# Performance work log

Hardware: AMD Instinct MI355X
Metric: run time of the kernel (lower is better)

## Reference

```python
import jax, jax.numpy as jnp
import numpy as np

N = 20000      # nodes
E = 320000     # edges (before self loops)
IN = 128       # in_channels
HID = 256      # hidden_channels
HEADS = 8
C = HID // HEADS  # 32 per-head dim
L = 4          # num_gat_layers
BN_EPS = 1e-5
LN_EPS = 1e-5


def setup_inputs() -> dict:
    key = jax.random.key(0)
    ks = iter(jax.random.split(key, 64))
    def rn(shape, s=0.05):
        return jax.random.normal(next(ks), shape, jnp.float32) * s
    inp = {
        'x': jax.random.normal(next(ks), (N, IN), jnp.float32),
        'edge_index': jax.random.randint(next(ks), (2, E), 0, N),
        # FeatureMLP
        'mlp_w1': rn((IN, HID)), 'mlp_b1': jnp.zeros((HID,), jnp.float32),
        'bn1_g': jnp.ones((HID,), jnp.float32), 'bn1_b': jnp.zeros((HID,), jnp.float32),
        'mlp_w2': rn((HID, HID)), 'mlp_b2': jnp.zeros((HID,), jnp.float32),
        'bn2_g': jnp.ones((HID,), jnp.float32), 'bn2_b': jnp.zeros((HID,), jnp.float32),
        'mlp_w3': rn((HID, HID)), 'mlp_b3': jnp.zeros((HID,), jnp.float32),
        # stacked GATv2 layer params [L, ...]
        'gat_wl': rn((L, HID, HID)), 'gat_bl': jnp.zeros((L, HID), jnp.float32),
        'gat_wr': rn((L, HID, HID)), 'gat_br': jnp.zeros((L, HID), jnp.float32),
        'gat_att': rn((L, HEADS, C)), 'gat_bias': jnp.zeros((L, HID), jnp.float32),
        'ln_g': jnp.ones((L, HID), jnp.float32), 'ln_b': jnp.zeros((L, HID), jnp.float32),
        'head_w1': rn((2 * HID, HID)), 'head_b1': jnp.zeros((HID,), jnp.float32),
        'hbn1_g': jnp.ones((HID,), jnp.float32), 'hbn1_b': jnp.zeros((HID,), jnp.float32),
        'head_w2': rn((HID, HID // 2)), 'head_b2': jnp.zeros((HID // 2,), jnp.float32),
        'hbn2_g': jnp.ones((HID // 2,), jnp.float32), 'hbn2_b': jnp.zeros((HID // 2,), jnp.float32),
        'head_w3': rn((HID // 2, HID // 4)), 'head_b3': jnp.zeros((HID // 4,), jnp.float32),
        'head_w4': rn((HID // 4, 1)), 'head_b4': jnp.zeros((1,), jnp.float32),
    }
    return inp


def _lrelu01(v):
    return jax.nn.leaky_relu(v, 0.1)


def _bn_eval(v, g, b):
    # eval-mode BatchNorm1d with running_mean=0, running_var=1
    return v * (g / jnp.sqrt(1.0 + BN_EPS)) + b


def _layernorm(v, g, b):
    mu = jnp.mean(v, axis=-1, keepdims=True)
    var = jnp.mean((v - mu) ** 2, axis=-1, keepdims=True)
    return (v - mu) / jnp.sqrt(var + LN_EPS) * g + b


def _gatv2(x, src, dst, Wl, bl, Wr, br, att, bias):
    n = x.shape[0]
    xl = (x @ Wl + bl).reshape(n, HEADS, C)   # source transform
    xr = (x @ Wr + br).reshape(n, HEADS, C)   # target transform
    # per-edge attention logits (GATv2): a . LeakyReLU(x_l[src] + x_r[dst])
    e = jax.nn.leaky_relu(xl[src] + xr[dst], 0.2)          # [E, H, C]
    logits = jnp.einsum('ehc,hc->eh', e, att)               # [E, H]
    # segment softmax over destination nodes
    m = jax.ops.segment_max(logits, dst, num_segments=n)    # [N, H]
    a = jnp.exp(logits - m[dst])
    s = jax.ops.segment_sum(a, dst, num_segments=n)
    alpha = a / (s[dst] + 1e-16)                            # [E, H]
    out = jax.ops.segment_sum(xl[src] * alpha[:, :, None], dst, num_segments=n)
    return out.reshape(n, HID) + bias


def _forward(x, mlp_w1, mlp_b1, bn1_g, bn1_b, mlp_w2, mlp_b2, bn2_g, bn2_b,
             mlp_w3, mlp_b3, gat_wl, gat_bl, gat_wr, gat_br, gat_att, gat_bias,
             ln_g, ln_b, head_w1, head_b1, hbn1_g, hbn1_b, head_w2, head_b2,
             hbn2_g, hbn2_b, head_w3, head_b3, head_w4, head_b4, edge_index):
    n = x.shape[0]
    # FeatureMLP (eval: dropout off)
    h = _lrelu01(_bn_eval(x @ mlp_w1 + mlp_b1, bn1_g, bn1_b))
    h = _lrelu01(_bn_eval(h @ mlp_w2 + mlp_b2, bn2_g, bn2_b))
    x_mlp = h @ mlp_w3 + mlp_b3
    # add self loops
    loop = jnp.arange(n)
    src = jnp.concatenate([edge_index[0], loop])
    dst = jnp.concatenate([edge_index[1], loop])
    g = x_mlp
    for i in range(L):
        res = g
        o = _gatv2(g, src, dst, gat_wl[i], gat_bl[i], gat_wr[i], gat_br[i],
                   gat_att[i], gat_bias[i])
        o = _lrelu01(_layernorm(o, ln_g[i], ln_b[i]))
        g = o + res
    xc = jnp.concatenate([x_mlp, g], axis=1)                # [N, 2*HID]
    h = _lrelu01(_bn_eval(xc @ head_w1 + head_b1, hbn1_g, hbn1_b))
    h = _lrelu01(_bn_eval(h @ head_w2 + head_b2, hbn2_g, hbn2_b))
    h = _lrelu01(h @ head_w3 + head_b3)
    return h @ head_w4 + head_b4                            # [N, 1]


def reference(x, edge_index, mlp_w1, mlp_b1, bn1_g, bn1_b, mlp_w2, mlp_b2,
              bn2_g, bn2_b, mlp_w3, mlp_b3, gat_wl, gat_bl, gat_wr, gat_br,
              gat_att, gat_bias, ln_g, ln_b, head_w1, head_b1, hbn1_g, hbn1_b,
              head_w2, head_b2, hbn2_g, hbn2_b, head_w3, head_b3, head_w4, head_b4):
    return _forward(x, mlp_w1, mlp_b1, bn1_g, bn1_b, mlp_w2, mlp_b2, bn2_g,
                    bn2_b, mlp_w3, mlp_b3, gat_wl, gat_bl, gat_wr, gat_br,
                    gat_att, gat_bias, ln_g, ln_b, head_w1, head_b1, hbn1_g,
                    hbn1_b, head_w2, head_b2, hbn2_g, hbn2_b, head_w3, head_b3,
                    head_w4, head_b4, edge_index)
```

## Files before the change

kernel.cpp:

```cpp
#include <hip/hip_runtime.h>
#include <hip/hip_bf16.h>

#define N_NODES 20000
#define E_EDGES 320000
#define E_TOT   (E_EDGES + N_NODES)
#define IN_CH   128
#define HID     256
#define HEADS   8
#define CPH     32

enum { EP_BIAS = 0, EP_BN_LRELU = 1, EP_LRELU = 2 };

typedef _Float16 f16;
typedef f16  f16x2 __attribute__((ext_vector_type(2)));
typedef f16  f16x4 __attribute__((ext_vector_type(4)));
typedef f16  f16x8 __attribute__((ext_vector_type(8)));
typedef float f32x2 __attribute__((ext_vector_type(2)));
typedef float f32x4 __attribute__((ext_vector_type(4)));

__device__ __forceinline__ f16x2 h2max(f16x2 a, f16x2 b) {
#if __has_builtin(__builtin_elementwise_max)
    return __builtin_elementwise_max(a, b);
#else
    f16x2 r; r[0] = a[0] > b[0] ? a[0] : b[0]; r[1] = a[1] > b[1] ? a[1] : b[1]; return r;
#endif
}
__device__ __forceinline__ float hdot2(f16x2 a, f16x2 b, float c) {
#if __has_builtin(__builtin_amdgcn_fdot2)
    return __builtin_amdgcn_fdot2(a, b, c, false);
#else
    return c + (float)a[0] * (float)b[0] + (float)a[1] * (float)b[1];
#endif
}
__device__ __forceinline__ float fexp2(float x) {
#if __has_builtin(__builtin_amdgcn_exp2f)
    return __builtin_amdgcn_exp2f(x);
#else
    return exp2f(x);
#endif
}

__device__ __forceinline__ size_t frag_idx(int row, int col, int KB) {
    int kb = col >> 6, ks = (col >> 5) & 1, q = (col >> 3) & 3, e = col & 7;
    return ((((size_t)(row >> 4) * KB + kb) * 2 + ks) << 9) + (((q << 4) | (row & 15)) << 3) + e;
}

struct WDesc { const float* src; f16* dst; int K; int Nc; int NTOT; int ct0; };
struct WDescs { WDesc d[14]; };

#define WPREP_BLKS (14 * 512)
#define CVT_BLKS   ((N_NODES * IN_CH) / 256)
#define DEG_BLKS   ((E_EDGES + 255) / 256)
#define ZERO_BLKS  ((N_NODES + 255) / 256)
#define PREP_BLKS  (WPREP_BLKS + CVT_BLKS + DEG_BLKS + ZERO_BLKS)

__global__ __launch_bounds__(256)
void prep_kernel(WDescs ds, const float* __restrict__ x, f16* __restrict__ x16,
                 const int* __restrict__ dstE, int* __restrict__ cnt, int* __restrict__ cur)
{
    const int bx = blockIdx.x;
    const int tid = threadIdx.x;
    if (bx < WPREP_BLKS) {
        WDesc w = ds.d[bx >> 9];
        int i = ((bx & 511) << 8) + tid;
        if (i < w.K * w.Nc) {
            int NT_local = w.Nc >> 4;
            int e  = i & 7;
            int l  = (i >> 3) & 63;
            int r  = i >> 9;
            int ct = r % NT_local;
            int q  = r / NT_local;
            int ks = q & 1;
            int kb = q >> 1;
            int n  = ct * 16 + (l & 15);
            int k  = kb * 64 + ks * 32 + ((l >> 4) << 3) + e;
            size_t di = (((size_t)(kb * 2 + ks) * w.NTOT + w.ct0 + ct) << 9) + (l << 3) + e;
            w.dst[di] = (f16)w.src[(size_t)k * w.Nc + n];
        }
    } else if (bx < WPREP_BLKS + CVT_BLKS) {
        int i = (bx - WPREP_BLKS) * 256 + tid;
        if (i < N_NODES * IN_CH) {
            int row = i / IN_CH, col = i - row * IN_CH;
            x16[frag_idx(row, col, 2)] = (f16)x[i];
        }
    } else if (bx < WPREP_BLKS + CVT_BLKS + DEG_BLKS) {
        int e = (bx - WPREP_BLKS - CVT_BLKS) * 256 + tid;
        if (e < E_EDGES) atomicAdd(&cnt[dstE[e]], 1);
    } else {
        int i = (bx - WPREP_BLKS - CVT_BLKS - DEG_BLKS) * 256 + tid;
        if (i < N_NODES) cur[i] = 0;
    }
}

template<int NT, int NTOT, int WAVES, int RT, int DOT, int OUTF>
__global__ __launch_bounds__(WAVES * 64)
void gemm_kernel(const f16* __restrict__ A1, int KB1,
                 const f16* __restrict__ A2, int KB2,
                 const f16* __restrict__ Wf,
                 const float* __restrict__ biasA,
                 const float* __restrict__ biasB,
                 const float* __restrict__ bng,
                 const float* __restrict__ bnb,
                 f16* __restrict__ out16A,
                 f16* __restrict__ out16B,
                 f16* __restrict__ dup16,
                 float* __restrict__ out32,
                 const float* __restrict__ dotw,
                 const float* __restrict__ dotb,
                 float* __restrict__ outdot,
                 int NcA, int KBo, int mode)
{
    __shared__ float red[DOT ? 16 : 1][DOT ? 65 : 1];
    const int tid  = threadIdx.x;
    const int wave = tid >> 6;
    const int lane = tid & 63;
    const int quad = lane >> 4;
    const int rb0 = blockIdx.x * RT;
    const int KBt = KB1 + KB2;

    f32x4 acc[RT][NT];
#pragma unroll
    for (int t = 0; t < RT; ++t)
#pragma unroll
        for (int j = 0; j < NT; ++j) acc[t][j] = (f32x4){0.f, 0.f, 0.f, 0.f};

#pragma unroll 2
    for (int kb = 0; kb < KBt; ++kb) {
#pragma unroll
        for (int ks = 0; ks < 2; ++ks) {
            f16x8 a[RT];
#pragma unroll
            for (int t = 0; t < RT; ++t) {
                const f16* ap = (kb < KB1)
                    ? A1 + (((((size_t)(rb0 + t)) * KB1 + kb) * 2 + ks) << 9) + (lane << 3)
                    : A2 + (((((size_t)(rb0 + t)) * KB2 + (kb - KB1)) * 2 + ks) << 9) + (lane << 3);
                a[t] = *(const f16x8*)ap;
            }
            const f16* bp = Wf + (((size_t)(kb * 2 + ks) * NTOT + wave * NT) << 9) + (lane << 3);
#pragma unroll
            for (int ct = 0; ct < NT; ++ct) {
                f16x8 b = *(const f16x8*)(bp + ((size_t)ct << 9));
#pragma unroll
                for (int t = 0; t < RT; ++t)
                    acc[t][ct] = __builtin_amdgcn_mfma_f32_16x16x32_f16(a[t], b, acc[t][ct], 0, 0, 0);
            }
        }
    }

    const int c0 = lane & 15;
    const int NcB = NTOT * 16 - NcA;
#pragma unroll
    for (int t = 0; t < RT; ++t) {
        const int r0 = (rb0 + t) * 16 + (quad << 2);
#pragma unroll
        for (int ct = 0; ct < NT; ++ct) {
            int col = (wave * NT + ct) * 16 + c0;
            bool isB = col >= NcA;
            int colL = isB ? col - NcA : col;
            float bv = isB ? biasB[colL] : biasA[colL];
            float sc = 1.f, sh = 0.f;
            if (mode == EP_BN_LRELU) {
                sc = bng[col] * rsqrtf(1.f + 1e-5f);
                sh = bnb[col];
            }
#pragma unroll
            for (int reg = 0; reg < 4; ++reg) {
                int row = r0 + reg;
                float v = acc[t][ct][reg] + bv;
                if (mode == EP_BN_LRELU) { v = v * sc + sh; v = v > 0.f ? v : 0.1f * v; }
                else if (mode == EP_LRELU) { v = v > 0.f ? v : 0.1f * v; }
                if (DOT) {
                    red[(quad << 2) + reg][col] = v * dotw[col];
                } else {
                    if (OUTF) {
                        size_t idx = frag_idx(row, col, KBo);
                        out16A[idx] = (f16)v;
                        if (dup16) dup16[idx] = (f16)v;
                        if (out32) out32[(size_t)row * NcA + col] = v;
                    } else {
                        f16* Cout = isB ? out16B : out16A;
                        int stride = isB ? NcB : NcA;
                        Cout[(size_t)row * stride + colL] = (f16)v;
                    }
                }
            }
        }
    }

    if (DOT) {
        __syncthreads();
        if (wave == 0) {
            int r = lane & 15, q = lane >> 4;
            float psum = 0.f;
#pragma unroll
            for (int j = 0; j < 16; ++j) psum += red[r][q * 16 + j];
            psum += __shfl_xor(psum, 16, 64);
            psum += __shfl_xor(psum, 32, 64);
            if (lane < 16) outdot[rb0 * 16 + r] = psum + dotb[0];
        }
    }
}

__global__ __launch_bounds__(512)
void head23_kernel(const f16* __restrict__ h1,
                   const f16* __restrict__ w2f,
                   const float* __restrict__ b2,
                   const float* __restrict__ bn2g, const float* __restrict__ bn2b,
                   const f16* __restrict__ w3f,
                   const float* __restrict__ b3,
                   const float* __restrict__ w4, const float* __restrict__ b4,
                   float* __restrict__ out)
{
    __shared__ f16  hs[32 * 136];
    __shared__ float red[32][65];
    const int tid  = threadIdx.x;
    const int wave = tid >> 6;
    const int lane = tid & 63;
    const int quad = lane >> 4;
    const int c0   = lane & 15;
    const int rb0  = blockIdx.x * 2;

    {
        f32x4 acc[2];
        acc[0] = (f32x4){0.f, 0.f, 0.f, 0.f};
        acc[1] = (f32x4){0.f, 0.f, 0.f, 0.f};
#pragma unroll
        for (int kb = 0; kb < 4; ++kb) {
#pragma unroll
            for (int ks = 0; ks < 2; ++ks) {
                f16x8 a0 = *(const f16x8*)(h1 + (((((size_t)rb0)     * 4 + kb) * 2 + ks) << 9) + (lane << 3));
                f16x8 a1 = *(const f16x8*)(h1 + (((((size_t)rb0 + 1) * 4 + kb) * 2 + ks) << 9) + (lane << 3));
                f16x8 b  = *(const f16x8*)(w2f + (((size_t)(kb * 2 + ks) * 8 + wave) << 9) + (lane << 3));
                acc[0] = __builtin_amdgcn_mfma_f32_16x16x32_f16(a0, b, acc[0], 0, 0, 0);
                acc[1] = __builtin_amdgcn_mfma_f32_16x16x32_f16(a1, b, acc[1], 0, 0, 0);
            }
        }
        const int col = wave * 16 + c0;
        const float sc = bn2g[col] * rsqrtf(1.f + 1e-5f);
        const float sh = bn2b[col];
        const float bv = b2[col];
#pragma unroll
        for (int t = 0; t < 2; ++t) {
            const int r0 = t * 16 + (quad << 2);
#pragma unroll
            for (int reg = 0; reg < 4; ++reg) {
                float v = acc[t][reg] + bv;
                v = v * sc + sh;
                v = v > 0.f ? v : 0.1f * v;
                hs[(r0 + reg) * 136 + col] = (f16)v;
            }
        }
    }
    __syncthreads();

    {
        const int rbL = wave >> 2;
        const int ct3 = wave & 3;
        f32x4 acc = (f32x4){0.f, 0.f, 0.f, 0.f};
#pragma unroll
        for (int ksl = 0; ksl < 4; ++ksl) {
            const int arow = rbL * 16 + (lane & 15);
            f16x8 a = *(const f16x8*)&hs[arow * 136 + ksl * 32 + ((lane >> 4) << 3)];
            f16x8 b = *(const f16x8*)(w3f + (((size_t)(ksl * 4 + ct3)) << 9) + (lane << 3));
            acc = __builtin_amdgcn_mfma_f32_16x16x32_f16(a, b, acc, 0, 0, 0);
        }
        const int col = ct3 * 16 + c0;
        const float wv = w4[col];
        const float bv = b3[col];
        const int r0 = rbL * 16 + (quad << 2);
#pragma unroll
        for (int reg = 0; reg < 4; ++reg) {
            float v = acc[reg] + bv;
            v = v > 0.f ? v : 0.1f * v;
            red[r0 + reg][col] = v * wv;
        }
    }
    __syncthreads();

    {
        const int row = wave * 4 + (lane >> 4);
        float pr = red[row][c0] + red[row][c0 + 16] + red[row][c0 + 32] + red[row][c0 + 48];
        pr += __shfl_xor(pr, 1, 64);
        pr += __shfl_xor(pr, 2, 64);
        pr += __shfl_xor(pr, 4, 64);
        pr += __shfl_xor(pr, 8, 64);
        if (c0 == 0) out[blockIdx.x * 32 + row] = pr + b4[0];
    }
}

__global__ __launch_bounds__(1024)
void scan_kernel(const int* __restrict__ cnt, int* __restrict__ off) {
    __shared__ int wsum[16];
    const int tid = threadIdx.x, wv = tid >> 6, ln = tid & 63;
    const int base = tid * 20;
    int pre[20];
    int loc = 0;
#pragma unroll
    for (int j = 0; j < 20; ++j) {
        int i = base + j;
        int c = (i < N_NODES) ? cnt[i] + 1 : 0;
        pre[j] = loc;
        loc += c;
    }
    int s = loc;
#pragma unroll
    for (int d = 1; d < 64; d <<= 1) { int t = __shfl_up(s, d, 64); if (ln >= d) s += t; }
    if (ln == 63) wsum[wv] = s;
    __syncthreads();
    int woff = 0;
#pragma unroll
    for (int j = 0; j < 16; ++j) if (j < wv) woff += wsum[j];
    int excl = woff + s - loc;
#pragma unroll
    for (int j = 0; j < 20; ++j) {
        int i = base + j;
        if (i < N_NODES) off[i] = excl + pre[j];
    }
    if (tid == 1023) off[N_NODES] = woff + s;
}

__global__ void fill_kernel(const int* __restrict__ src, const int* __restrict__ dst,
                            const int* __restrict__ off, int* __restrict__ cur, int* __restrict__ csr) {
    int i = blockIdx.x * 256 + threadIdx.x;
    if (i < E_EDGES) {
        int d = dst[i];
        int pos = atomicAdd(&cur[d], 1);
        csr[off[d] + pos] = src[i];
    } else {
        int j = i - E_EDGES;
        if (j < N_NODES) csr[off[j + 1] - 1] = j;
    }
}

__global__ __launch_bounds__(256)
void gat_agg_kernel(const f16* __restrict__ xl, const f16* __restrict__ xr,
                    float* __restrict__ g, f16* __restrict__ g16,
                    const int* __restrict__ off, const int* __restrict__ csr,
                    const float* __restrict__ att,
                    const float* __restrict__ bias,
                    const float* __restrict__ lng,
                    const float* __restrict__ lnb)
{
    const int wv   = threadIdx.x >> 6;
    const int ln   = threadIdx.x & 63;
    const int half = ln >> 5;
    const int lp   = ln & 31;
    const int n    = blockIdx.x * 4 + wv;
    if (n >= N_NODES) return;

    const f16x8* xl8 = (const f16x8*)xl;
    f16x8 xrv = ((const f16x8*)xr)[n * 32 + lp];
    f16x2 xr0; xr0[0] = xrv[0]; xr0[1] = xrv[1];
    f16x2 xr1; xr1[0] = xrv[2]; xr1[1] = xrv[3];
    f16x2 xr2; xr2[0] = xrv[4]; xr2[1] = xrv[5];
    f16x2 xr3; xr3[0] = xrv[6]; xr3[1] = xrv[7];
    float4 af0 = ((const float4*)att)[lp * 2];
    float4 af1 = ((const float4*)att)[lp * 2 + 1];
    const float L2E = 1.44269504f;
    f16x2 av0; av0[0] = (f16)(af0.x * L2E); av0[1] = (f16)(af0.y * L2E);
    f16x2 av1; av1[0] = (f16)(af0.z * L2E); av1[1] = (f16)(af0.w * L2E);
    f16x2 av2; av2[0] = (f16)(af1.x * L2E); av2[1] = (f16)(af1.y * L2E);
    f16x2 av3; av3[0] = (f16)(af1.z * L2E); av3[1] = (f16)(af1.w * L2E);
    const f16x2 k02 = { (f16)0.2f, (f16)0.2f };

    float s = 0.f;
    float o0 = 0.f, o1 = 0.f, o2 = 0.f, o3 = 0.f, o4 = 0.f, o5 = 0.f, o6 = 0.f, o7 = 0.f;

    int p = off[n], end = off[n + 1];

    auto procv = [&](f16x8 xv, bool valid) {
        f16x2 x0; x0[0] = xv[0]; x0[1] = xv[1];
        f16x2 x1; x1[0] = xv[2]; x1[1] = xv[3];
        f16x2 x2; x2[0] = xv[4]; x2[1] = xv[5];
        f16x2 x3; x3[0] = xv[6]; x3[1] = xv[7];
        f16x2 v0 = x0 + xr0, v1 = x1 + xr1, v2 = x2 + xr2, v3 = x3 + xr3;
        v0 = h2max(v0, v0 * k02); v1 = h2max(v1, v1 * k02);
        v2 = h2max(v2, v2 * k02); v3 = h2max(v3, v3 * k02);
        float pr = hdot2(v0, av0, hdot2(v1, av1, hdot2(v2, av2, hdot2(v3, av3, 0.f))));
        pr += __shfl_xor(pr, 1, 64);
        pr += __shfl_xor(pr, 2, 64);
        float e = valid ? fexp2(pr) : 0.f;
        s += e;
        o0 = fmaf((float)xv[0], e, o0); o1 = fmaf((float)xv[1], e, o1);
        o2 = fmaf((float)xv[2], e, o2); o3 = fmaf((float)xv[3], e, o3);
        o4 = fmaf((float)xv[4], e, o4); o5 = fmaf((float)xv[5], e, o5);
        o6 = fmaf((float)xv[6], e, o6); o7 = fmaf((float)xv[7], e, o7);
    };
    auto proc = [&](int ep) {
        bool valid = ep < end;
        int sidx = csr[valid ? ep : end - 1];
        procv(xl8[(size_t)sidx * 32 + lp], valid);
    };

    for (; p + 16 <= end; p += 16) {
        int sA = csr[p +      half];
        int sB = csr[p + 2  + half];
        int sC = csr[p + 4  + half];
        int sD = csr[p + 6  + half];
        int sE = csr[p + 8  + half];
        int sF = csr[p + 10 + half];
        int sG = csr[p + 12 + half];
        int sH = csr[p + 14 + half];
        f16x8 rA = xl8[(size_t)sA * 32 + lp];
        f16x8 rB = xl8[(size_t)sB * 32 + lp];
        f16x8 rC = xl8[(size_t)sC * 32 + lp];
        f16x8 rD = xl8[(size_t)sD * 32 + lp];
        f16x8 rE = xl8[(size_t)sE * 32 + lp];
        f16x8 rF = xl8[(size_t)sF * 32 + lp];
        f16x8 rG = xl8[(size_t)sG * 32 + lp];
        f16x8 rH = xl8[(size_t)sH * 32 + lp];
        procv(rA, true); procv(rB, true); procv(rC, true); procv(rD, true);
        procv(rE, true); procv(rF, true); procv(rG, true); procv(rH, true);
    }
    for (; p + 8 <= end; p += 8) {
        int sA = csr[p +     half];
        int sB = csr[p + 2 + half];
        int sC = csr[p + 4 + half];
        int sD = csr[p + 6 + half];
        f16x8 rA = xl8[(size_t)sA * 32 + lp];
        f16x8 rB = xl8[(size_t)sB * 32 + lp];
        f16x8 rC = xl8[(size_t)sC * 32 + lp];
        f16x8 rD = xl8[(size_t)sD * 32 + lp];
        procv(rA, true); procv(rB, true); procv(rC, true); procv(rD, true);
    }
    for (; p + 4 <= end; p += 4) {
        int sA = csr[p +     half];
        int sB = csr[p + 2 + half];
        f16x8 rA = xl8[(size_t)sA * 32 + lp];
        f16x8 rB = xl8[(size_t)sB * 32 + lp];
        procv(rA, true); procv(rB, true);
    }
    for (; p < end; p += 2) proc(p + half);

    s  += __shfl_xor(s, 32, 64);
    o0 += __shfl_xor(o0, 32, 64); o1 += __shfl_xor(o1, 32, 64);
    o2 += __shfl_xor(o2, 32, 64); o3 += __shfl_xor(o3, 32, 64);
    o4 += __shfl_xor(o4, 32, 64); o5 += __shfl_xor(o5, 32, 64);
    o6 += __shfl_xor(o6, 32, 64); o7 += __shfl_xor(o7, 32, 64);

    const int lidx = lp * 2 + half;
    float q0 = half ? o4 : o0;
    float q1 = half ? o5 : o1;
    float q2 = half ? o6 : o2;
    float q3 = half ? o7 : o3;

    float inv = 1.f / (s + 1e-16f);
    float4 bi = ((const float4*)bias)[lidx];
    float y0 = q0 * inv + bi.x;
    float y1 = q1 * inv + bi.y;
    float y2 = q2 * inv + bi.z;
    float y3 = q3 * inv + bi.w;

    float s1 = y0 + y1 + y2 + y3;
    float s2 = y0 * y0 + y1 * y1 + y2 * y2 + y3 * y3;
#pragma unroll
    for (int d = 32; d; d >>= 1) { s1 += __shfl_xor(s1, d, 64); s2 += __shfl_xor(s2, d, 64); }
    float mu  = s1 * (1.f / HID);
    float ex2 = s2 * (1.f / HID);
    float rstd = rsqrtf(ex2 - mu * mu + 1e-5f);
    float4 lg = ((const float4*)lng)[lidx];
    float4 lb = ((const float4*)lnb)[lidx];
    float nv0 = (y0 - mu) * rstd * lg.x + lb.x; nv0 = nv0 > 0.f ? nv0 : 0.1f * nv0;
    float nv1 = (y1 - mu) * rstd * lg.y + lb.y; nv1 = nv1 > 0.f ? nv1 : 0.1f * nv1;
    float nv2 = (y2 - mu) * rstd * lg.z + lb.z; nv2 = nv2 > 0.f ? nv2 : 0.1f * nv2;
    float nv3 = (y3 - mu) * rstd * lg.w + lb.w; nv3 = nv3 > 0.f ? nv3 : 0.1f * nv3;

    float4 gv = ((const float4*)g)[n * 64 + lidx];
    float g0 = nv0 + gv.x, g1 = nv1 + gv.y, g2 = nv2 + gv.z, g3 = nv3 + gv.w;
    ((float4*)g)[n * 64 + lidx] = make_float4(g0, g1, g2, g3);
    f16x4 gh; gh[0] = (f16)g0; gh[1] = (f16)g1; gh[2] = (f16)g2; gh[3] = (f16)g3;
    *(f16x4*)&g16[frag_idx(n, 4 * lidx, 4)] = gh;
}

static inline size_t align_up(size_t v, size_t a) { return (v + a - 1) & ~(a - 1); }

extern "C" void kernel_launch(void* const* d_in, const int* in_sizes, int n_in,
                              void* d_out, int out_size, void* d_ws, size_t ws_size,
                              hipStream_t stream)
{
    const float* x      = (const float*)d_in[0];
    const int*   ei     = (const int*)d_in[1];
    const float* mlp_w1 = (const float*)d_in[2];
    const float* mlp_b1 = (const float*)d_in[3];
    const float* bn1_g  = (const float*)d_in[4];
    const float* bn1_b  = (const float*)d_in[5];
    const float* mlp_w2 = (const float*)d_in[6];
    const float* mlp_b2 = (const float*)d_in[7];
    const float* bn2_g  = (const float*)d_in[8];
    const float* bn2_b  = (const float*)d_in[9];
    const float* mlp_w3 = (const float*)d_in[10];
    const float* mlp_b3 = (const float*)d_in[11];
    const float* gat_wl = (const float*)d_in[12];
    const float* gat_bl = (const float*)d_in[13];
    const float* gat_wr = (const float*)d_in[14];
    const float* gat_br = (const float*)d_in[15];
    const float* gat_att  = (const float*)d_in[16];
    const float* gat_bias = (const float*)d_in[17];
    const float* ln_g   = (const float*)d_in[18];
    const float* ln_b   = (const float*)d_in[19];
    const float* head_w1 = (const float*)d_in[20];
    const float* head_b1 = (const float*)d_in[21];
    const float* hbn1_g  = (const float*)d_in[22];
    const float* hbn1_b  = (const float*)d_in[23];
    const float* head_w2 = (const float*)d_in[24];
    const float* head_b2 = (const float*)d_in[25];
    const float* hbn2_g  = (const float*)d_in[26];
    const float* hbn2_b  = (const float*)d_in[27];
    const float* head_w3 = (const float*)d_in[28];
    const float* head_b3 = (const float*)d_in[29];
    const float* head_w4 = (const float*)d_in[30];
    const float* head_b4 = (const float*)d_in[31];
    float* out = (float*)d_out;

    char* w = (char*)d_ws;
    size_t p = 0;
    int* off  = (int*)(w + p); p = align_up(p + (N_NODES + 1) * sizeof(int), 64);
    int* fill = (int*)(w + p); p = align_up(p + N_NODES * sizeof(int), 64);
    int* cur  = (int*)(w + p); p = align_up(p + N_NODES * sizeof(int), 64);
    int* csr  = (int*)(w + p); p = align_up(p + E_TOT * sizeof(int), 64);
    float* g32 = (float*)(w + p); p = align_up(p + (size_t)N_NODES * HID * 4, 64);
    auto halloc = [&](size_t elems) {
        f16* q = (f16*)(w + p);
        p = align_up(p + elems * 2, 1024);
        return q;
    };
    f16* x16     = halloc((size_t)N_NODES * IN_CH);
    f16* h1      = halloc((size_t)N_NODES * HID);
    f16* h2      = halloc((size_t)N_NODES * HID);
    f16* x_mlp16 = halloc((size_t)N_NODES * HID);
    f16* g16     = halloc((size_t)N_NODES * HID);
    f16* xl16    = halloc((size_t)N_NODES * HID);
    f16* xr16    = halloc((size_t)N_NODES * HID);
    f16* wt_mlp1 = halloc((size_t)IN_CH * HID);
    f16* wt_mlp2 = halloc((size_t)HID * HID);
    f16* wt_mlp3 = halloc((size_t)HID * HID);
    f16* wt_g[4];
    for (int i = 0; i < 4; ++i) wt_g[i] = halloc((size_t)HID * 2 * HID);
    f16* wt_h1 = halloc((size_t)2 * HID * HID);
    f16* wt_h2 = halloc((size_t)HID * (HID / 2));
    f16* wt_h3 = halloc((size_t)(HID / 2) * (HID / 4));
    (void)ws_size; (void)in_sizes; (void)n_in; (void)out_size;

    const int* e_src = ei;
    const int* e_dst = ei + E_EDGES;

    dim3 blk(256);
    dim3 gM625((N_NODES + 31) / 32);

    WDescs ds;
    ds.d[0]  = { mlp_w1, wt_mlp1, IN_CH, HID, 16, 0 };
    ds.d[1]  = { mlp_w2, wt_mlp2, HID, HID, 16, 0 };
    ds.d[2]  = { mlp_w3, wt_mlp3, HID, HID, 16, 0 };
    for (int i = 0; i < 4; ++i) {
        ds.d[3 + 2 * i] = { gat_wl + (size_t)i * HID * HID, wt_g[i], HID, HID, 32, 0 };
        ds.d[4 + 2 * i] = { gat_wr + (size_t)i * HID * HID, wt_g[i], HID, HID, 32, 16 };
    }
    ds.d[11] = { head_w1, wt_h1, 2 * HID, HID, 16, 0 };
    ds.d[12] = { head_w2, wt_h2, HID, HID / 2, 8, 0 };
    ds.d[13] = { head_w3, wt_h3, HID / 2, HID / 4, 4, 0 };

    hipMemsetAsync(fill, 0, N_NODES * sizeof(int), stream);
    prep_kernel<<<dim3(PREP_BLKS), blk, 0, stream>>>(ds, x, x16, e_dst, fill, cur);
    scan_kernel<<<1, 1024, 0, stream>>>(fill, off);
    fill_kernel<<<(E_TOT + 255) / 256, blk, 0, stream>>>(e_src, e_dst, off, cur, csr);

    gemm_kernel<2, 16, 8, 2, 0, 1><<<gM625, 512, 0, stream>>>(x16, 2, nullptr, 0, wt_mlp1, mlp_b1, mlp_b1,
        bn1_g, bn1_b, h1, nullptr, nullptr, nullptr, nullptr, nullptr, nullptr, HID, 4, EP_BN_LRELU);
    gemm_kernel<2, 16, 8, 2, 0, 1><<<gM625, 512, 0, stream>>>(h1, 4, nullptr, 0, wt_mlp2, mlp_b2, mlp_b2,
        bn2_g, bn2_b, h2, nullptr, nullptr, nullptr, nullptr, nullptr, nullptr, HID, 4, EP_BN_LRELU);
    gemm_kernel<2, 16, 8, 2, 0, 1><<<gM625, 512, 0, stream>>>(h2, 4, nullptr, 0, wt_mlp3, mlp_b3, mlp_b3,
        nullptr, nullptr, x_mlp16, nullptr, g16, g32, nullptr, nullptr, nullptr, HID, 4, EP_BIAS);

    for (int i = 0; i < 4; ++i) {
        gemm_kernel<4, 32, 8, 2, 0, 0><<<gM625, 512, 0, stream>>>(g16, 4, nullptr, 0, wt_g[i],
            gat_bl + i * HID, gat_br + i * HID, nullptr, nullptr,
            xl16, xr16, nullptr, nullptr, nullptr, nullptr, nullptr, HID, 0, EP_BIAS);
        gat_agg_kernel<<<(N_NODES + 3) / 4, blk, 0, stream>>>(xl16, xr16, g32, g16, off, csr,
                                                              gat_att + i * HID, gat_bias + i * HID,
                                                              ln_g + i * HID, ln_b + i * HID);
    }

    gemm_kernel<2, 16, 8, 2, 0, 1><<<gM625, 512, 0, stream>>>(x_mlp16, 4, g16, 4, wt_h1, head_b1, head_b1,
        hbn1_g, hbn1_b, h1, nullptr, nullptr, nullptr, nullptr, nullptr, nullptr, HID, 4, EP_BN_LRELU);
    head23_kernel<<<gM625, 512, 0, stream>>>(h1, wt_h2, head_b2, hbn2_g, hbn2_b,
                                             wt_h3, head_b3, head_w4, head_b4, out);
}
```

Measured before the change: 445.6 us.

## Merge CSR scan/fill with the MLP1/MLP2 GEMMs and use nontemporal loads in aggregation

```diff
diff --git a/kernel.cpp b/kernel.cpp
--- a/kernel.cpp
+++ b/kernel.cpp
@@ -202,6 +202,165 @@
 }
 
 __global__ __launch_bounds__(512)
+void scan_mlp1_kernel(const int* __restrict__ cnt, int* __restrict__ off,
+                      const f16* __restrict__ x16, const f16* __restrict__ w1f,
+                      const float* __restrict__ b1,
+                      const float* __restrict__ bng, const float* __restrict__ bnb,
+                      f16* __restrict__ h1)
+{
+    __shared__ int wsum[8];
+    const int tid  = threadIdx.x;
+    const int wave = tid >> 6;
+    const int lane = tid & 63;
+
+    if (blockIdx.x == 0) {
+        const int base = tid * 40;
+        int pre[40];
+        int loc = 0;
+#pragma unroll
+        for (int j = 0; j < 40; ++j) {
+            int i = base + j;
+            int c = (i < N_NODES) ? cnt[i] + 1 : 0;
+            pre[j] = loc;
+            loc += c;
+        }
+        int s = loc;
+#pragma unroll
+        for (int d = 1; d < 64; d <<= 1) { int t = __shfl_up(s, d, 64); if (lane >= d) s += t; }
+        if (lane == 63) wsum[wave] = s;
+        __syncthreads();
+        int woff = 0;
+#pragma unroll
+        for (int j = 0; j < 8; ++j) if (j < wave) woff += wsum[j];
+        int excl = woff + s - loc;
+#pragma unroll
+        for (int j = 0; j < 40; ++j) {
+            int i = base + j;
+            if (i < N_NODES) off[i] = excl + pre[j];
+        }
+        if (tid == 511) off[N_NODES] = woff + s;
+        return;
+    }
+
+    const int quad = lane >> 4;
+    const int c0   = lane & 15;
+    const int rb0  = (blockIdx.x - 1) * 2;
+    f32x4 acc[2][2];
+#pragma unroll
+    for (int t = 0; t < 2; ++t)
+#pragma unroll
+        for (int j = 0; j < 2; ++j) acc[t][j] = (f32x4){0.f, 0.f, 0.f, 0.f};
+#pragma unroll
+    for (int kb = 0; kb < 2; ++kb) {
+#pragma unroll
+        for (int ks = 0; ks < 2; ++ks) {
+            f16x8 a[2];
+#pragma unroll
+            for (int t = 0; t < 2; ++t)
+                a[t] = *(const f16x8*)(x16 + (((((size_t)(rb0 + t)) * 2 + kb) * 2 + ks) << 9) + (lane << 3));
+            const f16* bp = w1f + (((size_t)(kb * 2 + ks) * 16 + wave * 2) << 9) + (lane << 3);
+#pragma unroll
+            for (int ct = 0; ct < 2; ++ct) {
+                f16x8 b = *(const f16x8*)(bp + ((size_t)ct << 9));
+#pragma unroll
+                for (int t = 0; t < 2; ++t)
+                    acc[t][ct] = __builtin_amdgcn_mfma_f32_16x16x32_f16(a[t], b, acc[t][ct], 0, 0, 0);
+            }
+        }
+    }
+#pragma unroll
+    for (int t = 0; t < 2; ++t) {
+        const int r0 = (rb0 + t) * 16 + (quad << 2);
+#pragma unroll
+        for (int ct = 0; ct < 2; ++ct) {
+            const int col = (wave * 2 + ct) * 16 + c0;
+            const float sc = bng[col] * rsqrtf(1.f + 1e-5f);
+            const float sh = bnb[col];
+            const float bv = b1[col];
+#pragma unroll
+            for (int reg = 0; reg < 4; ++reg) {
+                float v = acc[t][ct][reg] + bv;
+                v = v * sc + sh;
+                v = v > 0.f ? v : 0.1f * v;
+                h1[frag_idx(r0 + reg, col, 4)] = (f16)v;
+            }
+        }
+    }
+}
+
+#define FILL_BLKS ((E_TOT + 511) / 512)
+
+__global__ __launch_bounds__(512)
+void fill_mlp2_kernel(const int* __restrict__ src, const int* __restrict__ dst,
+                      const int* __restrict__ off, int* __restrict__ cur, int* __restrict__ csr,
+                      const f16* __restrict__ h1, const f16* __restrict__ w2f,
+                      const float* __restrict__ b2,
+                      const float* __restrict__ bng, const float* __restrict__ bnb,
+                      f16* __restrict__ h2)
+{
+    const int tid  = threadIdx.x;
+    if (blockIdx.x < FILL_BLKS) {
+        int i = blockIdx.x * 512 + tid;
+        if (i < E_EDGES) {
+            int d = dst[i];
+            int pos = atomicAdd(&cur[d], 1);
+            csr[off[d] + pos] = src[i];
+        } else if (i < E_TOT) {
+            int j = i - E_EDGES;
+            csr[off[j + 1] - 1] = j;
+        }
+        return;
+    }
+
+    const int wave = tid >> 6;
+    const int lane = tid & 63;
+    const int quad = lane >> 4;
+    const int c0   = lane & 15;
+    const int rb0  = (blockIdx.x - FILL_BLKS) * 2;
+    f32x4 acc[2][2];
+#pragma unroll
+    for (int t = 0; t < 2; ++t)
+#pragma unroll
+        for (int j = 0; j < 2; ++j) acc[t][j] = (f32x4){0.f, 0.f, 0.f, 0.f};
+#pragma unroll
+    for (int kb = 0; kb < 4; ++kb) {
+#pragma unroll
+        for (int ks = 0; ks < 2; ++ks) {
+            f16x8 a[2];
+#pragma unroll
+            for (int t = 0; t < 2; ++t)
+                a[t] = *(const f16x8*)(h1 + (((((size_t)(rb0 + t)) * 4 + kb) * 2 + ks) << 9) + (lane << 3));
+            const f16* bp = w2f + (((size_t)(kb * 2 + ks) * 16 + wave * 2) << 9) + (lane << 3);
+#pragma unroll
+            for (int ct = 0; ct < 2; ++ct) {
+                f16x8 b = *(const f16x8*)(bp + ((size_t)ct << 9));
+#pragma unroll
+                for (int t = 0; t < 2; ++t)
+                    acc[t][ct] = __builtin_amdgcn_mfma_f32_16x16x32_f16(a[t], b, acc[t][ct], 0, 0, 0);
+            }
+        }
+    }
+#pragma unroll
+    for (int t = 0; t < 2; ++t) {
+        const int r0 = (rb0 + t) * 16 + (quad << 2);
+#pragma unroll
+        for (int ct = 0; ct < 2; ++ct) {
+            const int col = (wave * 2 + ct) * 16 + c0;
+            const float sc = bng[col] * rsqrtf(1.f + 1e-5f);
+            const float sh = bnb[col];
+            const float bv = b2[col];
+#pragma unroll
+            for (int reg = 0; reg < 4; ++reg) {
+                float v = acc[t][ct][reg] + bv;
+                v = v * sc + sh;
+                v = v > 0.f ? v : 0.1f * v;
+                h2[frag_idx(r0 + reg, col, 4)] = (f16)v;
+            }
+        }
+    }
+}
+
+__global__ __launch_bounds__(512)
 void head23_kernel(const f16* __restrict__ h1,
                    const f16* __restrict__ w2f,
                    const float* __restrict__ b2,
@@ -288,50 +447,6 @@
     }
 }
 
-__global__ __launch_bounds__(1024)
-void scan_kernel(const int* __restrict__ cnt, int* __restrict__ off) {
-    __shared__ int wsum[16];
-    const int tid = threadIdx.x, wv = tid >> 6, ln = tid & 63;
-    const int base = tid * 20;
-    int pre[20];
-    int loc = 0;
-#pragma unroll
-    for (int j = 0; j < 20; ++j) {
-        int i = base + j;
-        int c = (i < N_NODES) ? cnt[i] + 1 : 0;
-        pre[j] = loc;
-        loc += c;
-    }
-    int s = loc;
-#pragma unroll
-    for (int d = 1; d < 64; d <<= 1) { int t = __shfl_up(s, d, 64); if (ln >= d) s += t; }
-    if (ln == 63) wsum[wv] = s;
-    __syncthreads();
-    int woff = 0;
-#pragma unroll
-    for (int j = 0; j < 16; ++j) if (j < wv) woff += wsum[j];
-    int excl = woff + s - loc;
-#pragma unroll
-    for (int j = 0; j < 20; ++j) {
-        int i = base + j;
-        if (i < N_NODES) off[i] = excl + pre[j];
-    }
-    if (tid == 1023) off[N_NODES] = woff + s;
-}
-
-__global__ void fill_kernel(const int* __restrict__ src, const int* __restrict__ dst,
-                            const int* __restrict__ off, int* __restrict__ cur, int* __restrict__ csr) {
-    int i = blockIdx.x * 256 + threadIdx.x;
-    if (i < E_EDGES) {
-        int d = dst[i];
-        int pos = atomicAdd(&cur[d], 1);
-        csr[off[d] + pos] = src[i];
-    } else {
-        int j = i - E_EDGES;
-        if (j < N_NODES) csr[off[j + 1] - 1] = j;
-    }
-}
-
 __global__ __launch_bounds__(256)
 void gat_agg_kernel(const f16* __restrict__ xl, const f16* __restrict__ xr,
                     float* __restrict__ g, f16* __restrict__ g16,
@@ -349,7 +464,7 @@
     if (n >= N_NODES) return;
 
     const f16x8* xl8 = (const f16x8*)xl;
-    f16x8 xrv = ((const f16x8*)xr)[n * 32 + lp];
+    f16x8 xrv = __builtin_nontemporal_load((const f16x8*)xr + n * 32 + lp);
     f16x2 xr0; xr0[0] = xrv[0]; xr0[1] = xrv[1];
     f16x2 xr1; xr1[0] = xrv[2]; xr1[1] = xrv[3];
     f16x2 xr2; xr2[0] = xrv[4]; xr2[1] = xrv[5];
@@ -465,9 +580,10 @@
     float nv2 = (y2 - mu) * rstd * lg.z + lb.z; nv2 = nv2 > 0.f ? nv2 : 0.1f * nv2;
     float nv3 = (y3 - mu) * rstd * lg.w + lb.w; nv3 = nv3 > 0.f ? nv3 : 0.1f * nv3;
 
-    float4 gv = ((const float4*)g)[n * 64 + lidx];
-    float g0 = nv0 + gv.x, g1 = nv1 + gv.y, g2 = nv2 + gv.z, g3 = nv3 + gv.w;
-    ((float4*)g)[n * 64 + lidx] = make_float4(g0, g1, g2, g3);
+    f32x4 gv = __builtin_nontemporal_load((const f32x4*)g + n * 64 + lidx);
+    float g0 = nv0 + gv[0], g1 = nv1 + gv[1], g2 = nv2 + gv[2], g3 = nv3 + gv[3];
+    f32x4 gw; gw[0] = g0; gw[1] = g1; gw[2] = g2; gw[3] = g3;
+    __builtin_nontemporal_store(gw, (f32x4*)g + n * 64 + lidx);
     f16x4 gh; gh[0] = (f16)g0; gh[1] = (f16)g1; gh[2] = (f16)g2; gh[3] = (f16)g3;
     *(f16x4*)&g16[frag_idx(n, 4 * lidx, 4)] = gh;
 }
@@ -561,13 +677,12 @@
 
     hipMemsetAsync(fill, 0, N_NODES * sizeof(int), stream);
     prep_kernel<<<dim3(PREP_BLKS), blk, 0, stream>>>(ds, x, x16, e_dst, fill, cur);
-    scan_kernel<<<1, 1024, 0, stream>>>(fill, off);
-    fill_kernel<<<(E_TOT + 255) / 256, blk, 0, stream>>>(e_src, e_dst, off, cur, csr);
-
-    gemm_kernel<2, 16, 8, 2, 0, 1><<<gM625, 512, 0, stream>>>(x16, 2, nullptr, 0, wt_mlp1, mlp_b1, mlp_b1,
-        bn1_g, bn1_b, h1, nullptr, nullptr, nullptr, nullptr, nullptr, nullptr, HID, 4, EP_BN_LRELU);
-    gemm_kernel<2, 16, 8, 2, 0, 1><<<gM625, 512, 0, stream>>>(h1, 4, nullptr, 0, wt_mlp2, mlp_b2, mlp_b2,
-        bn2_g, bn2_b, h2, nullptr, nullptr, nullptr, nullptr, nullptr, nullptr, HID, 4, EP_BN_LRELU);
+
+    scan_mlp1_kernel<<<dim3(1 + 625), dim3(512), 0, stream>>>(fill, off, x16, wt_mlp1,
+        mlp_b1, bn1_g, bn1_b, h1);
+    fill_mlp2_kernel<<<dim3(FILL_BLKS + 625), dim3(512), 0, stream>>>(e_src, e_dst, off, cur, csr,
+        h1, wt_mlp2, mlp_b2, bn2_g, bn2_b, h2);
+
     gemm_kernel<2, 16, 8, 2, 0, 1><<<gM625, 512, 0, stream>>>(h2, 4, nullptr, 0, wt_mlp3, mlp_b3, mlp_b3,
         nullptr, nullptr, x_mlp16, nullptr, g16, g32, nullptr, nullptr, nullptr, HID, 4, EP_BIAS);
 
```

Result: slower. 462.7 us (+3.8%).
